# Performance work log

Measured on AMD Instinct MI355X. Metric: run time of the kernel, lower is better.

Reference implementation:

```python
import jax, jax.numpy as jnp
import numpy as np

B, DIM, HEADS, H, W = 4, 64, 64, 256, 256


def _conv1x1(x, w):
    # x: [b,c,h,w], w: [o,c] -> [b,o,h,w]
    return jnp.einsum('bchw,oc->bohw', x, w)


def _conv3x3_s2_reflect(x, w, groups):
    # reflect pad 1, 3x3 conv, stride 2 (matches padding_mode='reflect', stride=2)
    xp = jnp.pad(x, ((0, 0), (0, 0), (1, 1), (1, 1)), mode='reflect')
    return jax.lax.conv_general_dilated(
        xp, w, window_strides=(2, 2), padding='VALID',
        dimension_numbers=('NCHW', 'OIHW', 'NCHW'), feature_group_count=groups)


def _to_heads(t, heads):
    # safe_rearrange: zero-pad channels to a multiple of heads, then b (head c) h w -> b head c (h w)
    b, c, h, w = t.shape
    if c % heads != 0:
        t = jnp.pad(t, ((0, 0), (0, heads - c % heads), (0, 0), (0, 0)))
        c = t.shape[1]
    return t.reshape(b, heads, c // heads, h * w)


def _l2norm(t, eps=1e-12):
    # F.normalize(dim=-1): x / max(||x||, eps)
    n = jnp.sqrt(jnp.sum(t * t, axis=-1, keepdims=True))
    return t / jnp.maximum(n, eps)


def setup_inputs() -> dict:
    key = jax.random.key(0)
    ks = jax.random.split(key, 13)
    d = DIM
    s = 0.05
    return {
        'x': jax.random.normal(ks[0], (B, d, H, W), jnp.float32),
        'illu_feat': jax.random.uniform(ks[1], (B, d, H, W), jnp.float32),
        'w_q_spec': jax.random.normal(ks[2], (d, d), jnp.float32) * s,
        'w_k_spec': jax.random.normal(ks[3], (d, d), jnp.float32) * s,
        'w_v_spec': jax.random.normal(ks[4], (d, d), jnp.float32) * s,
        'w_q_spat': jax.random.normal(ks[5], (d, 1, 3, 3), jnp.float32) * s,  # depthwise
        'w_k_spat': jax.random.normal(ks[6], (d, d, 3, 3), jnp.float32) * s,
        'w_v_spat': jax.random.normal(ks[7], (d, d), jnp.float32) * s,
        'w_anchor_dw': jax.random.normal(ks[8], (d, 1, 3, 3), jnp.float32) * s,  # depthwise
        'w_anchor_pw': jax.random.normal(ks[9], (d // 2, d), jnp.float32) * s,
        'w_proj': jax.random.normal(ks[10], (d, d), jnp.float32) * s,
        'temp_spec': jnp.ones((HEADS, 1, 1), jnp.float32),
        'temp_spat': jnp.ones((HEADS, 1, 1), jnp.float32),
    }


def reference(x, illu_feat, w_q_spec, w_k_spec, w_v_spec, w_q_spat, w_k_spat,
              w_v_spat, w_anchor_dw, w_anchor_pw, w_proj, temp_spec, temp_spat):
    b, c, h, w = x.shape
    heads = HEADS

    q_spec = _conv1x1(x, w_q_spec)
    k_spec = _conv1x1(x, w_k_spec)                       # computed but unused downstream (as in original)
    v_spec = _conv1x1(x, w_v_spec) * illu_feat
    q_spat = _conv3x3_s2_reflect(x, w_q_spat, groups=c)  # computed but unused downstream (as in original)
    k_spat = _conv3x3_s2_reflect(x, w_k_spat, groups=1)
    v_spat = _conv1x1(x, w_v_spat) * illu_feat
    anchor = _conv1x1(_conv3x3_s2_reflect(x, w_anchor_dw, groups=c), w_anchor_pw)

    q_spec = _l2norm(_to_heads(q_spec, heads))
    k_spec = _l2norm(_to_heads(k_spec, heads))
    v_spec = _to_heads(v_spec, heads)
    q_spat = _l2norm(_to_heads(q_spat, heads))
    k_spat = _to_heads(k_spat, heads)
    v_spat = _to_heads(v_spat, heads)
    anchor = _l2norm(_to_heads(anchor, heads))

    n_q = q_spec.shape[-1]      # h*w
    n_a = anchor.shape[-1]      # (h//2)*(w//2)
    n_v = v_spec.shape[-1]
    n_k = k_spat.shape[-1]

    # spectral branch: q x anchor (truncate to common spatial length)
    m = min(n_q, n_a)
    attn_spec = jnp.einsum('bhcn,bhdn->bhcd', q_spec[..., :m], anchor[..., :m]) * temp_spec
    attn_spec = jax.nn.softmax(attn_spec, axis=-1)

    # v_spec spatial matching via adaptive avg pool (static no-op here since n_v == n_q)
    if n_v != n_q:
        vh = int(n_v ** 0.5)
        qh = int(n_q ** 0.5)
        v4 = v_spec.reshape(b, heads, v_spec.shape[2], vh, vh)
        v4 = jax.image.resize(v4, (b, heads, v_spec.shape[2], qh, qh), method='linear')
        v_spec_matched = v4.reshape(b, heads, v_spec.shape[2], -1)
    else:
        v_spec_matched = v_spec

    # spatial branch: anchor x k_spat (truncate to common spatial length)
    m2 = min(n_a, n_k)
    attn_spat = jnp.einsum('bhcn,bhdn->bhcd', anchor[..., :m2], k_spat[..., :m2]) * temp_spat
    attn_spat = jax.nn.softmax(attn_spat, axis=-1)

    out_spec = jnp.einsum('bhcd,bhdn->bhcn', attn_spec, v_spec_matched)
    out_spat = jnp.einsum('bhcd,bhdn->bhcn', attn_spat, v_spat)

    m3 = min(out_spec.shape[-1], out_spat.shape[-1])
    out = 0.6 * out_spec[..., :m3] + 0.4 * out_spat[..., :m3]

    ah = int(m3 ** 0.5)
    out = out.reshape(b, heads * out.shape[2], ah, ah)
    if ah != h or ah != w:
        # F.interpolate bilinear, align_corners=False == half-pixel linear resize
        out = jax.image.resize(out, (b, out.shape[1], h, w), method='bilinear')
    out = out[:, :DIM]
    return _conv1x1(out, w_proj)
```

## Files before the change

### kernel.cpp

```cpp
#include <hip/hip_runtime.h>


#define HW 65536
#define CH 64
#define PT 128
#define SX 68

typedef short s4_t __attribute__((ext_vector_type(4)));
typedef short s8_t __attribute__((ext_vector_type(8)));
typedef float f4_t __attribute__((ext_vector_type(4)));

static __device__ __forceinline__ unsigned short f2bf(float f) {
  unsigned u = __float_as_uint(f);
  return (unsigned short)((u + 0x7fffu + ((u >> 16) & 1u)) >> 16);
}
static __device__ __forceinline__ s8_t ld8(const unsigned short* p) {
  s4_t lo = *(const s4_t*)p;
  s4_t hi = *(const s4_t*)(p + 4);
  s8_t r = {lo[0], lo[1], lo[2], lo[3], hi[0], hi[1], hi[2], hi[3]};
  return r;
}

__global__ __launch_bounds__(256, 4) void fused_hsattn(
    const float* __restrict__ x, const float* __restrict__ illu,
    const float* __restrict__ wvs, const float* __restrict__ wvt,
    const float* __restrict__ wproj, float* __restrict__ out) {
  __shared__ __align__(16) unsigned short XH[PT * SX];
  __shared__ __align__(16) unsigned short WM[CH * SX];
  __shared__ __align__(16) unsigned short WP[CH * SX];

  const int tid  = threadIdx.x;
  const int bb   = blockIdx.x >> 9;
  const int pix0 = (blockIdx.x & 511) << 7;
  const int base = bb * CH * HW + pix0;

#pragma unroll
  for (int it = 0; it < 4; ++it) {
    int idx = it * 256 + tid;
    int j4  = idx * 4;
    int row = idx >> 4, col = (idx & 15) * 4;
    f4_t a = *(const f4_t*)(wvs + j4);
    f4_t b = *(const f4_t*)(wvt + j4);
    f4_t p = *(const f4_t*)(wproj + j4);
    s4_t m, w;
#pragma unroll
    for (int j = 0; j < 4; ++j) {
      m[j] = (short)f2bf(0.6f * a[j] + 0.4f * b[j]);
      w[j] = (short)f2bf(p[j]);
    }
    *(s4_t*)(WM + row * SX + col) = m;
    *(s4_t*)(WP + row * SX + col) = w;
  }

  {
    const int ch = tid & 63, ps = tid >> 6;
    const float* xp = x + base + ch * HW + ps * 32;
#pragma unroll
    for (int k = 0; k < 8; ++k) {
      f4_t v = *(const f4_t*)(xp + k * 4);
#pragma unroll
      for (int j = 0; j < 4; ++j)
        XH[(ps * 32 + k * 4 + j) * SX + ch] = f2bf(v[j]);
    }
  }
  __syncthreads();

  const int lane = tid & 63;
  const int wv   = tid >> 6;
  const int n15  = lane & 15, q = lane >> 4;
  const int nb   = wv * 32;

  f4_t acc[8];
#pragma unroll
  for (int i = 0; i < 8; ++i) acc[i] = (f4_t){0.f, 0.f, 0.f, 0.f};
#pragma unroll
  for (int kc = 0; kc < 2; ++kc) {
    s8_t A[4];
#pragma unroll
    for (int mt = 0; mt < 4; ++mt)
      A[mt] = ld8(WM + (mt * 16 + n15) * SX + kc * 32 + q * 8);
#pragma unroll
    for (int nt = 0; nt < 2; ++nt) {
      s8_t B = ld8(XH + (nb + nt * 16 + n15) * SX + kc * 32 + q * 8);
#pragma unroll
      for (int mt = 0; mt < 4; ++mt)
        acc[mt * 2 + nt] =
            __builtin_amdgcn_mfma_f32_16x16x32_bf16(A[mt], B, acc[mt * 2 + nt], 0, 0, 0);
    }
  }

  s4_t uh[8];
#pragma unroll
  for (int mt = 0; mt < 4; ++mt)
#pragma unroll
    for (int nt = 0; nt < 2; ++nt) {
      const float* ip = illu + base + (mt * 16 + q * 4) * HW + nb + nt * 16 + n15;
      f4_t a = acc[mt * 2 + nt];
      s4_t h;
#pragma unroll
      for (int r = 0; r < 4; ++r) h[r] = (short)f2bf(a[r] * ip[r * HW]);
      uh[mt * 2 + nt] = h;
    }
  __syncthreads();

#pragma unroll
  for (int mt = 0; mt < 4; ++mt)
#pragma unroll
    for (int nt = 0; nt < 2; ++nt)
      *(s4_t*)(XH + (nb + nt * 16 + n15) * SX + mt * 16 + q * 4) = uh[mt * 2 + nt];
  __syncthreads();

  f4_t acc2[8];
#pragma unroll
  for (int i = 0; i < 8; ++i) acc2[i] = (f4_t){0.f, 0.f, 0.f, 0.f};
#pragma unroll
  for (int kc = 0; kc < 2; ++kc) {
    s8_t A[4];
#pragma unroll
    for (int mt = 0; mt < 4; ++mt)
      A[mt] = ld8(WP + (mt * 16 + n15) * SX + kc * 32 + q * 8);
#pragma unroll
    for (int nt = 0; nt < 2; ++nt) {
      s8_t B = ld8(XH + (nb + nt * 16 + n15) * SX + kc * 32 + q * 8);
#pragma unroll
      for (int mt = 0; mt < 4; ++mt)
        acc2[mt * 2 + nt] =
            __builtin_amdgcn_mfma_f32_16x16x32_bf16(A[mt], B, acc2[mt * 2 + nt], 0, 0, 0);
    }
  }

#pragma unroll
  for (int mt = 0; mt < 4; ++mt)
#pragma unroll
    for (int nt = 0; nt < 2; ++nt) {
      float* op = out + base + (mt * 16 + q * 4) * HW + nb + nt * 16 + n15;
      f4_t a = acc2[mt * 2 + nt];
#pragma unroll
      for (int r = 0; r < 4; ++r) op[r * HW] = a[r];
    }
}

extern "C" void kernel_launch(void* const* d_in, const int* in_sizes, int n_in,
                              void* d_out, int out_size, void* d_ws, size_t ws_size,
                              hipStream_t stream) {
  const float* x     = (const float*)d_in[0];
  const float* illu  = (const float*)d_in[1];
  const float* wvs   = (const float*)d_in[4];
  const float* wvt   = (const float*)d_in[7];
  const float* wproj = (const float*)d_in[10];
  float* out = (float*)d_out;

  fused_hsattn<<<4 * (HW / PT), 256, 0, stream>>>(x, illu, wvs, wvt, wproj, out);
}
```

Measured before the change: 201.6 us.

## Stage x and illu tiles into LDS via async global_load_lds with 64-pixel tiles

Halves the pixel tile per block to 64 and loads both x and illu tiles directly into shared memory with global_load_lds, which bypasses registers. The illu multiply now reads from LDS rather than doing strided global loads in the epilogue. Each wave owns a private 16-pixel slice, so the barriers around the intermediate write-back are removed. In exchange LDS use grows (two fp32 64x64 tiles), the occupancy hint drops to 2 blocks, and the grid doubles, so weight conversion is repeated by twice as many blocks.

Result: no change. 198.2 us (-1.7%).

```diff
diff --git a/kernel.cpp b/kernel.cpp
--- a/kernel.cpp
+++ b/kernel.cpp
@@ -3,12 +3,15 @@
 
 #define HW 65536
 #define CH 64
-#define PT 128
+#define PT 64
 #define SX 68
 
 typedef short s4_t __attribute__((ext_vector_type(4)));
 typedef short s8_t __attribute__((ext_vector_type(8)));
 typedef float f4_t __attribute__((ext_vector_type(4)));
+
+typedef const __attribute__((address_space(1))) unsigned int* gp_t;
+typedef __attribute__((address_space(3))) unsigned int* lp_t;
 
 static __device__ __forceinline__ unsigned short f2bf(float f) {
   unsigned u = __float_as_uint(f);
@@ -20,124 +23,124 @@
   s8_t r = {lo[0], lo[1], lo[2], lo[3], hi[0], hi[1], hi[2], hi[3]};
   return r;
 }
+static __device__ __forceinline__ void gload16(const float* g, float* l) {
+  __builtin_amdgcn_global_load_lds((gp_t)(unsigned long long)g,
+                                   (lp_t)(unsigned long long)l, 16, 0, 0);
+}
 
-__global__ __launch_bounds__(256, 4) void fused_hsattn(
+__global__ __launch_bounds__(256, 2) void fused_hsattn(
     const float* __restrict__ x, const float* __restrict__ illu,
     const float* __restrict__ wvs, const float* __restrict__ wvt,
     const float* __restrict__ wproj, float* __restrict__ out) {
+  __shared__ __align__(16) float xs[CH * PT];
+  __shared__ __align__(16) float ils[CH * PT];
   __shared__ __align__(16) unsigned short XH[PT * SX];
   __shared__ __align__(16) unsigned short WM[CH * SX];
   __shared__ __align__(16) unsigned short WP[CH * SX];
 
   const int tid  = threadIdx.x;
-  const int bb   = blockIdx.x >> 9;
-  const int pix0 = (blockIdx.x & 511) << 7;
+  const int bb   = blockIdx.x >> 10;
+  const int pix0 = (blockIdx.x & 1023) << 6;
   const int base = bb * CH * HW + pix0;
+  const int lane = tid & 63;
+  const int wv   = tid >> 6;
+
+  f4_t wa[4], wb[4], wc[4];
+#pragma unroll
+  for (int it = 0; it < 4; ++it) {
+    int j4 = (it * 256 + tid) * 4;
+    wa[it] = *(const f4_t*)(wvs + j4);
+    wb[it] = *(const f4_t*)(wvt + j4);
+    wc[it] = *(const f4_t*)(wproj + j4);
+  }
+
+#pragma unroll
+  for (int it = 0; it < 4; ++it) {
+    int u = wv * 1024 + it * 256;
+    int f = u + lane * 4;
+    int c = f >> 6, p = f & 63;
+    gload16(x + base + c * HW + p, xs + u);
+    gload16(illu + base + c * HW + p, ils + u);
+  }
 
 #pragma unroll
   for (int it = 0; it < 4; ++it) {
     int idx = it * 256 + tid;
-    int j4  = idx * 4;
-    int row = idx >> 4, col = (idx & 15) * 4;
-    f4_t a = *(const f4_t*)(wvs + j4);
-    f4_t b = *(const f4_t*)(wvt + j4);
-    f4_t p = *(const f4_t*)(wproj + j4);
+    int r = idx >> 4, c4 = (idx & 15) * 4;
     s4_t m, w;
 #pragma unroll
     for (int j = 0; j < 4; ++j) {
-      m[j] = (short)f2bf(0.6f * a[j] + 0.4f * b[j]);
-      w[j] = (short)f2bf(p[j]);
+      m[j] = (short)f2bf(0.6f * wa[it][j] + 0.4f * wb[it][j]);
+      w[j] = (short)f2bf(wc[it][j]);
     }
-    *(s4_t*)(WM + row * SX + col) = m;
-    *(s4_t*)(WP + row * SX + col) = w;
+    *(s4_t*)(WM + r * SX + c4) = m;
+    *(s4_t*)(WP + r * SX + c4) = w;
   }
+  __syncthreads();
 
   {
-    const int ch = tid & 63, ps = tid >> 6;
-    const float* xp = x + base + ch * HW + ps * 32;
+    const int p = tid & 63, cc = (tid >> 6) << 4;
 #pragma unroll
-    for (int k = 0; k < 8; ++k) {
-      f4_t v = *(const f4_t*)(xp + k * 4);
-#pragma unroll
-      for (int j = 0; j < 4; ++j)
-        XH[(ps * 32 + k * 4 + j) * SX + ch] = f2bf(v[j]);
+    for (int k = 0; k < 16; k += 2) {
+      float f0 = xs[(cc + k) * PT + p];
+      float f1 = xs[(cc + k + 1) * PT + p];
+      unsigned pk = (unsigned)f2bf(f0) | ((unsigned)f2bf(f1) << 16);
+      *(unsigned*)(XH + p * SX + cc + k) = pk;
     }
   }
   __syncthreads();
 
-  const int lane = tid & 63;
-  const int wv   = tid >> 6;
-  const int n15  = lane & 15, q = lane >> 4;
-  const int nb   = wv * 32;
+  const int n15 = lane & 15, q = lane >> 4;
+  const int nb  = wv * 16;
 
-  f4_t acc[8];
+  f4_t acc[4];
 #pragma unroll
-  for (int i = 0; i < 8; ++i) acc[i] = (f4_t){0.f, 0.f, 0.f, 0.f};
+  for (int i = 0; i < 4; ++i) acc[i] = (f4_t){0.f, 0.f, 0.f, 0.f};
 #pragma unroll
   for (int kc = 0; kc < 2; ++kc) {
-    s8_t A[4];
+    s8_t B = ld8(XH + (nb + n15) * SX + kc * 32 + q * 8);
 #pragma unroll
-    for (int mt = 0; mt < 4; ++mt)
-      A[mt] = ld8(WM + (mt * 16 + n15) * SX + kc * 32 + q * 8);
-#pragma unroll
-    for (int nt = 0; nt < 2; ++nt) {
-      s8_t B = ld8(XH + (nb + nt * 16 + n15) * SX + kc * 32 + q * 8);
-#pragma unroll
-      for (int mt = 0; mt < 4; ++mt)
-        acc[mt * 2 + nt] =
-            __builtin_amdgcn_mfma_f32_16x16x32_bf16(A[mt], B, acc[mt * 2 + nt], 0, 0, 0);
+    for (int mt = 0; mt < 4; ++mt) {
+      s8_t A = ld8(WM + (mt * 16 + n15) * SX + kc * 32 + q * 8);
+      acc[mt] = __builtin_amdgcn_mfma_f32_16x16x32_bf16(A, B, acc[mt], 0, 0, 0);
     }
   }
 
-  s4_t uh[8];
+  s4_t uh[4];
+#pragma unroll
+  for (int mt = 0; mt < 4; ++mt) {
+    s4_t h;
+#pragma unroll
+    for (int r = 0; r < 4; ++r) {
+      int c = mt * 16 + q * 4 + r;
+      h[r] = (short)f2bf(acc[mt][r] * ils[c * PT + nb + n15]);
+    }
+    uh[mt] = h;
+  }
 #pragma unroll
   for (int mt = 0; mt < 4; ++mt)
+    *(s4_t*)(XH + (nb + n15) * SX + mt * 16 + q * 4) = uh[mt];
+
+  f4_t acc2[4];
 #pragma unroll
-    for (int nt = 0; nt < 2; ++nt) {
-      const float* ip = illu + base + (mt * 16 + q * 4) * HW + nb + nt * 16 + n15;
-      f4_t a = acc[mt * 2 + nt];
-      s4_t h;
-#pragma unroll
-      for (int r = 0; r < 4; ++r) h[r] = (short)f2bf(a[r] * ip[r * HW]);
-      uh[mt * 2 + nt] = h;
-    }
-  __syncthreads();
-
-#pragma unroll
-  for (int mt = 0; mt < 4; ++mt)
-#pragma unroll
-    for (int nt = 0; nt < 2; ++nt)
-      *(s4_t*)(XH + (nb + nt * 16 + n15) * SX + mt * 16 + q * 4) = uh[mt * 2 + nt];
-  __syncthreads();
-
-  f4_t acc2[8];
-#pragma unroll
-  for (int i = 0; i < 8; ++i) acc2[i] = (f4_t){0.f, 0.f, 0.f, 0.f};
+  for (int i = 0; i < 4; ++i) acc2[i] = (f4_t){0.f, 0.f, 0.f, 0.f};
 #pragma unroll
   for (int kc = 0; kc < 2; ++kc) {
-    s8_t A[4];
+    s8_t B = ld8(XH + (nb + n15) * SX + kc * 32 + q * 8);
 #pragma unroll
-    for (int mt = 0; mt < 4; ++mt)
-      A[mt] = ld8(WP + (mt * 16 + n15) * SX + kc * 32 + q * 8);
-#pragma unroll
-    for (int nt = 0; nt < 2; ++nt) {
-      s8_t B = ld8(XH + (nb + nt * 16 + n15) * SX + kc * 32 + q * 8);
-#pragma unroll
-      for (int mt = 0; mt < 4; ++mt)
-        acc2[mt * 2 + nt] =
-            __builtin_amdgcn_mfma_f32_16x16x32_bf16(A[mt], B, acc2[mt * 2 + nt], 0, 0, 0);
+    for (int mt = 0; mt < 4; ++mt) {
+      s8_t A = ld8(WP + (mt * 16 + n15) * SX + kc * 32 + q * 8);
+      acc2[mt] = __builtin_amdgcn_mfma_f32_16x16x32_bf16(A, B, acc2[mt], 0, 0, 0);
     }
   }
 
 #pragma unroll
-  for (int mt = 0; mt < 4; ++mt)
+  for (int mt = 0; mt < 4; ++mt) {
+    float* op = out + base + (mt * 16 + q * 4) * HW + nb + n15;
+    f4_t a = acc2[mt];
 #pragma unroll
-    for (int nt = 0; nt < 2; ++nt) {
-      float* op = out + base + (mt * 16 + q * 4) * HW + nb + nt * 16 + n15;
-      f4_t a = acc2[mt * 2 + nt];
-#pragma unroll
-      for (int r = 0; r < 4; ++r) op[r * HW] = a[r];
-    }
+    for (int r = 0; r < 4; ++r) op[r * HW] = a[r];
+  }
 }
 
 extern "C" void kernel_launch(void* const* d_in, const int* in_sizes, int n_in,
```
